# Kernel tuning notes

Hardware: AMD Instinct MI355X
Metric: run time of the kernel (lower is better)

Reference implementation:

```python
import jax, jax.numpy as jnp
import numpy as np

B, N, M = 2, 131072, 512
VOXEL_SIZE = 0.5
SCALE = 10.0          # points lie in [0, SCALE)^3
G = 20                # static voxels per axis: ceil(SCALE / VOXEL_SIZE)
V = G * G * G         # total voxels per batch element


def setup_inputs() -> dict:
    key = jax.random.key(0)
    kx, ks = jax.random.split(key)
    x = jax.random.uniform(kx, (B, N, 3), dtype=jnp.float32) * SCALE
    # random_sample_point_cloud: sample M point indices without replacement per batch
    perm = jax.vmap(lambda k: jax.random.permutation(k, N))(jax.random.split(ks, B))
    sampled_idx = perm[:, :M].astype(jnp.int32)
    return {"x": x, "sampled_idx": sampled_idx}


def _voxel_idx(pts, min_coords):
    # metric_to_voxel_space: floor((p - min) / voxel_size), clipped to the grid
    idx = jnp.floor((pts - min_coords[:, None, :]) / VOXEL_SIZE).astype(jnp.int32)
    return jnp.clip(idx, 0, G - 1)  # (B, n, 3)


def reference(x, sampled_idx):
    # --- estimate_normal_distributions_with_size: per-voxel mean + covariance ---
    min_coords = x.min(axis=1)                                     # (B, 3)
    vox = _voxel_idx(x, min_coords)                                # (B, N, 3)
    flat = (vox[..., 0] * G + vox[..., 1]) * G + vox[..., 2]       # (B, N) flat voxel id

    seg = (flat + jnp.arange(B, dtype=flat.dtype)[:, None] * V).reshape(-1)  # global seg ids
    pts = x.reshape(-1, 3)
    cnt = jax.ops.segment_sum(jnp.ones((B * N,), jnp.float32), seg,
                              num_segments=B * V).reshape(B, V, 1)
    s1 = jax.ops.segment_sum(pts, seg, num_segments=B * V).reshape(B, V, 3)
    outer = (pts[:, :, None] * pts[:, None, :]).reshape(-1, 9)
    s2 = jax.ops.segment_sum(outer, seg, num_segments=B * V).reshape(B, V, 9)

    safe = jnp.maximum(cnt, 1.0)                                   # empty voxels -> zeros
    mean = s1 / safe                                               # (B, V, 3)
    cov = s2 / safe - (mean[:, :, :, None] * mean[:, :, None, :]).reshape(B, V, 9)
    dists = jnp.concatenate([mean, cov], axis=-1)                  # (B, V, 12)

    # --- gather distributions at the sampled points' voxels ---
    sflat = jnp.take_along_axis(flat, sampled_idx.astype(jnp.int32), axis=1)   # (B, M)
    filtered = jnp.take_along_axis(dists, sflat[..., None], axis=1)            # (B, M, 12)
    return filtered
```

## Files before the change

kernel.cpp:

```cpp
#include <hip/hip_runtime.h>

#define BB 2
#define NN 131072
#define MM 512
#define GG 20
#define VV (GG * GG * GG)
#define NBLKX 128

#define OFF_PARTIAL 0
#define OFF_SUMS    4096
#define ZI4         (640000 / 16)

__device__ __forceinline__ int vox_coord(float p, float mn) {
    int i = (int)floorf((p - mn) * 2.0f);
    return min(max(i, 0), GG - 1);
}

__device__ __forceinline__ void reduce_min_prologue(const char* ws, int b, int t,
                                                    float* smin) {
    if (t < 192) {
        const int axis = t >> 6, lane = t & 63;
        const float* pm = (const float*)(ws + OFF_PARTIAL);
        float m = fminf(pm[(b * NBLKX + lane) * 3 + axis],
                        pm[(b * NBLKX + lane + 64) * 3 + axis]);
        for (int off = 32; off > 0; off >>= 1)
            m = fminf(m, __shfl_down(m, off, 64));
        if (lane == 0) smin[axis] = m;
    }
}

__global__ __launch_bounds__(256) void vox_min(const float* __restrict__ x,
                                               char* __restrict__ ws) {
    const int b = blockIdx.y;
    const int tid = blockIdx.x * 256 + threadIdx.x;
    const int gtid = (b * NBLKX + blockIdx.x) * 256 + threadIdx.x;

    {
        int4* z = (int4*)(ws + OFF_SUMS);
        if (gtid < ZI4) z[gtid] = make_int4(0, 0, 0, 0);
    }

    const float4* xb = (const float4*)(x + (size_t)b * NN * 3);
    float4 f0 = xb[3 * tid + 0];
    float4 f1 = xb[3 * tid + 1];
    float4 f2 = xb[3 * tid + 2];
    float mx = fminf(fminf(f0.x, f0.w), fminf(f1.z, f2.y));
    float my = fminf(fminf(f0.y, f1.x), fminf(f1.w, f2.z));
    float mz = fminf(fminf(f0.z, f1.y), fminf(f2.x, f2.w));

    for (int off = 32; off > 0; off >>= 1) {
        mx = fminf(mx, __shfl_down(mx, off, 64));
        my = fminf(my, __shfl_down(my, off, 64));
        mz = fminf(mz, __shfl_down(mz, off, 64));
    }
    __shared__ float lmin[4][3];
    int wave = threadIdx.x >> 6;
    if ((threadIdx.x & 63) == 0) {
        lmin[wave][0] = mx; lmin[wave][1] = my; lmin[wave][2] = mz;
    }
    __syncthreads();
    if (threadIdx.x == 0) {
        float* pm = (float*)(ws + OFF_PARTIAL) + (b * NBLKX + blockIdx.x) * 3;
        pm[0] = fminf(fminf(lmin[0][0], lmin[1][0]), fminf(lmin[2][0], lmin[3][0]));
        pm[1] = fminf(fminf(lmin[0][1], lmin[1][1]), fminf(lmin[2][1], lmin[3][1]));
        pm[2] = fminf(fminf(lmin[0][2], lmin[1][2]), fminf(lmin[2][2], lmin[3][2]));
    }
}

__global__ __launch_bounds__(256) void vox_accum(const float* __restrict__ x,
                                                 const int* __restrict__ sidx,
                                                 char* __restrict__ ws) {
    const int b = blockIdx.y;
    const int t = threadIdx.x;
    const int tid = blockIdx.x * 256 + t;

    __shared__ float smin[3];
    __shared__ unsigned int bm[250];

    if (t < 250) bm[t] = 0u;
    reduce_min_prologue(ws, b, t, smin);
    __syncthreads();
    const float mnx = smin[0], mny = smin[1], mnz = smin[2];

#pragma unroll
    for (int k = 0; k < 2; ++k) {
        const int j = t + k * 256;
        const int pi = sidx[b * MM + j];
        const float* p = x + ((size_t)b * NN + pi) * 3;
        int ix = vox_coord(p[0], mnx);
        int iy = vox_coord(p[1], mny);
        int iz = vox_coord(p[2], mnz);
        int flat = (ix * GG + iy) * GG + iz;
        atomicOr(&bm[flat >> 5], 1u << (flat & 31));
    }
    __syncthreads();

    float* sums = (float*)(ws + OFF_SUMS) + (size_t)b * VV * 10;
    const float4* xb = (const float4*)(x + (size_t)b * NN * 3);
    float4 f0 = xb[3 * tid + 0];
    float4 f1 = xb[3 * tid + 1];
    float4 f2 = xb[3 * tid + 2];
    float px[4] = {f0.x, f0.w, f1.z, f2.y};
    float py[4] = {f0.y, f1.x, f1.w, f2.z};
    float pz[4] = {f0.z, f1.y, f2.x, f2.w};
#pragma unroll
    for (int k = 0; k < 4; ++k) {
        int ix = vox_coord(px[k], mnx);
        int iy = vox_coord(py[k], mny);
        int iz = vox_coord(pz[k], mnz);
        int flat = (ix * GG + iy) * GG + iz;
        if ((bm[flat >> 5] >> (flat & 31)) & 1u) {
            float* s = sums + (size_t)flat * 10;
            unsafeAtomicAdd(s + 0, 1.0f);
            unsafeAtomicAdd(s + 1, px[k]);
            unsafeAtomicAdd(s + 2, py[k]);
            unsafeAtomicAdd(s + 3, pz[k]);
            unsafeAtomicAdd(s + 4, px[k] * px[k]);
            unsafeAtomicAdd(s + 5, px[k] * py[k]);
            unsafeAtomicAdd(s + 6, px[k] * pz[k]);
            unsafeAtomicAdd(s + 7, py[k] * py[k]);
            unsafeAtomicAdd(s + 8, py[k] * pz[k]);
            unsafeAtomicAdd(s + 9, pz[k] * pz[k]);
        }
    }
}

__global__ __launch_bounds__(512) void vox_final(const float* __restrict__ x,
                                                 const int* __restrict__ sidx,
                                                 const char* __restrict__ ws,
                                                 float* __restrict__ out) {
    const int b = blockIdx.x;
    const int t = threadIdx.x;

    __shared__ float smin[3];
    reduce_min_prologue(ws, b, t, smin);
    __syncthreads();

    const int pi = sidx[b * MM + t];
    const float* p = x + ((size_t)b * NN + pi) * 3;
    int ix = vox_coord(p[0], smin[0]);
    int iy = vox_coord(p[1], smin[1]);
    int iz = vox_coord(p[2], smin[2]);
    int flat = (ix * GG + iy) * GG + iz;

    const float* s = (const float*)(ws + OFF_SUMS) + ((size_t)b * VV + flat) * 10;
    float cnt = s[0];
    float inv = 1.0f / fmaxf(cnt, 1.0f);
    float mx = s[1] * inv, my = s[2] * inv, mz = s[3] * inv;
    float cxx = s[4] * inv - mx * mx;
    float cxy = s[5] * inv - mx * my;
    float cxz = s[6] * inv - mx * mz;
    float cyy = s[7] * inv - my * my;
    float cyz = s[8] * inv - my * mz;
    float czz = s[9] * inv - mz * mz;
    float* o = out + (size_t)(b * MM + t) * 12;
    o[0] = mx;  o[1] = my;  o[2] = mz;
    o[3] = cxx; o[4] = cxy; o[5] = cxz;
    o[6] = cxy; o[7] = cyy; o[8] = cyz;
    o[9] = cxz; o[10] = cyz; o[11] = czz;
}

extern "C" void kernel_launch(void* const* d_in, const int* in_sizes, int n_in,
                              void* d_out, int out_size, void* d_ws, size_t ws_size,
                              hipStream_t stream) {
    const float* x = (const float*)d_in[0];
    const int* sidx = (const int*)d_in[1];
    float* out = (float*)d_out;
    char* ws = (char*)d_ws;

    vox_min<<<dim3(NBLKX, BB), 256, 0, stream>>>(x, ws);
    vox_accum<<<dim3(NBLKX, BB), 256, 0, stream>>>(x, sidx, ws);
    vox_final<<<BB, 512, 0, stream>>>(x, sidx, ws, out);
}
```

Measured before the change: 77.65 us.

## Fuse final gather into accumulate kernel via last-block atomic counter

Removes the separate finalize kernel by having the last block to finish accumulation (detected with an atomic counter plus threadfence) compute means/covariances for both batches. Accumulate blocks grow to 512 threads and compute the min for both batches. This saves a kernel launch and its dependency gap, at the cost of a serialized tail on a single block and extra fences.

```diff
diff --git a/kernel.cpp b/kernel.cpp
--- a/kernel.cpp
+++ b/kernel.cpp
@@ -6,27 +6,16 @@
 #define GG 20
 #define VV (GG * GG * GG)
 #define NBLKX 128
+#define NBLK2 64
 
 #define OFF_PARTIAL 0
+#define OFF_CTR     4080
 #define OFF_SUMS    4096
-#define ZI4         (640000 / 16)
+#define ZI4         ((16 + 640000) / 16)
 
 __device__ __forceinline__ int vox_coord(float p, float mn) {
     int i = (int)floorf((p - mn) * 2.0f);
     return min(max(i, 0), GG - 1);
-}
-
-__device__ __forceinline__ void reduce_min_prologue(const char* ws, int b, int t,
-                                                    float* smin) {
-    if (t < 192) {
-        const int axis = t >> 6, lane = t & 63;
-        const float* pm = (const float*)(ws + OFF_PARTIAL);
-        float m = fminf(pm[(b * NBLKX + lane) * 3 + axis],
-                        pm[(b * NBLKX + lane + 64) * 3 + axis]);
-        for (int off = 32; off > 0; off >>= 1)
-            m = fminf(m, __shfl_down(m, off, 64));
-        if (lane == 0) smin[axis] = m;
-    }
 }
 
 __global__ __launch_bounds__(256) void vox_min(const float* __restrict__ x,
@@ -36,7 +25,7 @@
     const int gtid = (b * NBLKX + blockIdx.x) * 256 + threadIdx.x;
 
     {
-        int4* z = (int4*)(ws + OFF_SUMS);
+        int4* z = (int4*)(ws + OFF_CTR);
         if (gtid < ZI4) z[gtid] = make_int4(0, 0, 0, 0);
     }
 
@@ -67,25 +56,34 @@
     }
 }
 
-__global__ __launch_bounds__(256) void vox_accum(const float* __restrict__ x,
+__global__ __launch_bounds__(512) void vox_accum(const float* __restrict__ x,
                                                  const int* __restrict__ sidx,
-                                                 char* __restrict__ ws) {
+                                                 char* __restrict__ ws,
+                                                 float* __restrict__ out) {
     const int b = blockIdx.y;
     const int t = threadIdx.x;
-    const int tid = blockIdx.x * 256 + t;
+    const int tid = blockIdx.x * 512 + t;
 
-    __shared__ float smin[3];
+    __shared__ float smin[BB][3];
     __shared__ unsigned int bm[250];
+    __shared__ int lastFlag;
 
     if (t < 250) bm[t] = 0u;
-    reduce_min_prologue(ws, b, t, smin);
+    if (t < 384) {
+        const int pair = t >> 6, lane = t & 63;
+        const int pb = pair / 3, axis = pair % 3;
+        const float* pm = (const float*)(ws + OFF_PARTIAL);
+        float m = fminf(pm[(pb * NBLKX + lane) * 3 + axis],
+                        pm[(pb * NBLKX + lane + 64) * 3 + axis]);
+        for (int off = 32; off > 0; off >>= 1)
+            m = fminf(m, __shfl_down(m, off, 64));
+        if (lane == 0) smin[pb][axis] = m;
+    }
     __syncthreads();
-    const float mnx = smin[0], mny = smin[1], mnz = smin[2];
+    const float mnx = smin[b][0], mny = smin[b][1], mnz = smin[b][2];
 
-#pragma unroll
-    for (int k = 0; k < 2; ++k) {
-        const int j = t + k * 256;
-        const int pi = sidx[b * MM + j];
+    {
+        const int pi = sidx[b * MM + t];
         const float* p = x + ((size_t)b * NN + pi) * 3;
         int ix = vox_coord(p[0], mnx);
         int iy = vox_coord(p[1], mny);
@@ -123,41 +121,40 @@
             unsafeAtomicAdd(s + 9, pz[k] * pz[k]);
         }
     }
-}
 
-__global__ __launch_bounds__(512) void vox_final(const float* __restrict__ x,
-                                                 const int* __restrict__ sidx,
-                                                 const char* __restrict__ ws,
-                                                 float* __restrict__ out) {
-    const int b = blockIdx.x;
-    const int t = threadIdx.x;
+    __threadfence();
+    if (t == 0)
+        lastFlag = (atomicAdd((int*)(ws + OFF_CTR), 1) == NBLK2 * BB - 1);
+    __syncthreads();
+    if (!lastFlag) return;
 
-    __shared__ float smin[3];
-    reduce_min_prologue(ws, b, t, smin);
-    __syncthreads();
-
-    const int pi = sidx[b * MM + t];
-    const float* p = x + ((size_t)b * NN + pi) * 3;
-    int ix = vox_coord(p[0], smin[0]);
-    int iy = vox_coord(p[1], smin[1]);
-    int iz = vox_coord(p[2], smin[2]);
-    int flat = (ix * GG + iy) * GG + iz;
-
-    const float* s = (const float*)(ws + OFF_SUMS) + ((size_t)b * VV + flat) * 10;
-    float cnt = s[0];
-    float inv = 1.0f / fmaxf(cnt, 1.0f);
-    float mx = s[1] * inv, my = s[2] * inv, mz = s[3] * inv;
-    float cxx = s[4] * inv - mx * mx;
-    float cxy = s[5] * inv - mx * my;
-    float cxz = s[6] * inv - mx * mz;
-    float cyy = s[7] * inv - my * my;
-    float cyz = s[8] * inv - my * mz;
-    float czz = s[9] * inv - mz * mz;
-    float* o = out + (size_t)(b * MM + t) * 12;
-    o[0] = mx;  o[1] = my;  o[2] = mz;
-    o[3] = cxx; o[4] = cxy; o[5] = cxz;
-    o[6] = cxy; o[7] = cyy; o[8] = cyz;
-    o[9] = cxz; o[10] = cyz; o[11] = czz;
+    __threadfence();
+#pragma unroll
+    for (int k = 0; k < 2; ++k) {
+        const int j = t + k * 512;
+        const int fb = j >> 9;
+        const int pi = sidx[fb * MM + (j & (MM - 1))];
+        const float* p = x + ((size_t)fb * NN + pi) * 3;
+        int ix = vox_coord(p[0], smin[fb][0]);
+        int iy = vox_coord(p[1], smin[fb][1]);
+        int iz = vox_coord(p[2], smin[fb][2]);
+        int flat = (ix * GG + iy) * GG + iz;
+        const float* s = (const float*)(ws + OFF_SUMS) + ((size_t)fb * VV + flat) * 10;
+        float cnt = s[0];
+        float inv = 1.0f / fmaxf(cnt, 1.0f);
+        float mx = s[1] * inv, my = s[2] * inv, mz = s[3] * inv;
+        float cxx = s[4] * inv - mx * mx;
+        float cxy = s[5] * inv - mx * my;
+        float cxz = s[6] * inv - mx * mz;
+        float cyy = s[7] * inv - my * my;
+        float cyz = s[8] * inv - my * mz;
+        float czz = s[9] * inv - mz * mz;
+        float* o = out + (size_t)j * 12;
+        o[0] = mx;  o[1] = my;  o[2] = mz;
+        o[3] = cxx; o[4] = cxy; o[5] = cxz;
+        o[6] = cxy; o[7] = cyy; o[8] = cyz;
+        o[9] = cxz; o[10] = cyz; o[11] = czz;
+    }
 }
 
 extern "C" void kernel_launch(void* const* d_in, const int* in_sizes, int n_in,
@@ -169,6 +166,5 @@
     char* ws = (char*)d_ws;
 
     vox_min<<<dim3(NBLKX, BB), 256, 0, stream>>>(x, ws);
-    vox_accum<<<dim3(NBLKX, BB), 256, 0, stream>>>(x, sidx, ws);
-    vox_final<<<BB, 512, 0, stream>>>(x, sidx, ws, out);
+    vox_accum<<<dim3(NBLK2, BB), 512, 0, stream>>>(x, sidx, ws, out);
 }
```

After: 88.54 us. 1.14x slower.
